# Optimization experiments

Hardware: AMD Instinct MI355X
Metric: run time of the kernel (lower is better)

The kernel has to match this reference:

```python
import jax, jax.numpy as jnp
import numpy as np

B, N, L, E, D = 16, 16384, 192, 128, 128


def setup_inputs() -> dict:
    key = jax.random.key(0)
    ks = jax.random.split(key, 16)
    s = 0.05
    return {
        "x_L_flattened": jax.random.normal(ks[0], (B, N), jnp.float32),
        "x_y_mask_flattened": jax.random.randint(ks[1], (B, N), 0, 2).astype(jnp.float32),
        "y_mask_L_flattened": jnp.zeros((B, N), jnp.float32),
        "x_y_mark": jax.random.normal(ks[2], (B, L, 1), jnp.float32),
        "variable_indices_flattened": jax.random.randint(ks[3], (B, N), 0, E),
        "time_indices_flattened": jax.random.randint(ks[4], (B, N), 0, L),
        "N_OBSERVATIONS_MAX": N,
        # learned params (stored [in, out]; torch Linear uses x @ W.T + b)
        "W_obs": jax.random.normal(ks[5], (2, D), jnp.float32) * s,
        "b_obs": jnp.zeros((D,), jnp.float32),
        "W_time": jax.random.normal(ks[6], (1, D), jnp.float32) * s,
        "b_time": jnp.zeros((D,), jnp.float32),
        "var_hyperedge_w": jax.random.normal(ks[7], (E, D), jnp.float32),
        "W_q": jax.random.normal(ks[8], (D, D), jnp.float32) * s,
        "b_q": jnp.zeros((D,), jnp.float32),
        "W_k": jax.random.normal(ks[9], (D, D), jnp.float32) * s,
        "b_k": jnp.zeros((D,), jnp.float32),
        "W_v": jax.random.normal(ks[10], (D, D), jnp.float32) * s,
        "b_v": jnp.zeros((D,), jnp.float32),
        "threshold": jnp.float32(0.5),
        "merge_coef": jnp.float32(0.5),
    }


def reference(x_L_flattened, x_y_mask_flattened, y_mask_L_flattened, x_y_mark,
              variable_indices_flattened, time_indices_flattened, N_OBSERVATIONS_MAX,
              W_obs, b_obs, W_time, b_time, var_hyperedge_w,
              W_q, b_q, W_k, b_k, W_v, b_v, threshold, merge_coef):
    mask = x_y_mask_flattened  # [B, N]
    # node features: value + (1 - mask + y_mask) channel -> [B, N, 2]
    feats = jnp.stack([x_L_flattened, 1.0 - mask + y_mask_L_flattened], axis=-1)
    # temporal incidence: node n belongs to time-edge l iff time_idx[n] == l; [B, L, N]
    ti = (time_indices_flattened[:, None, :] == jnp.arange(L)[None, :, None]).astype(jnp.float32)
    ti = ti * mask[:, None, :]
    # variable incidence: node n belongs to var-edge e iff var_idx[n] == e; [B, E, N]
    vi = (jnp.arange(E)[None, :, None] == variable_indices_flattened[:, None, :]).astype(jnp.float32)
    vi = vi * mask[:, None, :]
    # encoders
    obs = jax.nn.relu(feats @ W_obs + b_obs) * mask[..., None]          # [B, N, D]
    temp_he = jnp.sin(x_y_mark @ W_time + b_time)                        # [B, L, D]
    var_he = jax.nn.relu(jnp.broadcast_to(var_hyperedge_w, (B, E, D)))   # [B, E, D]
    # IrregularityAwareAttention over variable hyperedges with incidence as aux
    q = var_he @ W_q + b_q
    k = var_he @ W_k + b_k
    v = var_he @ W_v + b_v
    att = jnp.einsum('bed,bfd->bef', q, k) / (D ** 0.5)                  # [B, E, E]
    att_aux = jnp.einsum('ben,bfn->bef', vi, vi) / (N_OBSERVATIONS_MAX ** 0.5)
    merge = (att > threshold) & (att_aux != 0)
    att = jnp.where(merge, (1.0 - merge_coef) * att + merge_coef * att_aux, att)
    attn = jax.nn.softmax(att, axis=-1)
    out = jnp.einsum('bef,bfd->bed', attn, v)                            # [B, E, D]
    return (obs, temp_he, out, ti, vi)
```

## Files before the change

### kernel.cpp

```cpp
#include <hip/hip_runtime.h>

#define Bb 16
#define Nn 16384
#define Ll 192
#define Ee 128
#define Dd 128


#define QKV_NB   128
#define TEMP_NB  512
#define FILL_NB  2048
#define OBS_NB   2048
#define TEMP_B0  (QKV_NB)
#define FILL_B0  (TEMP_B0 + TEMP_NB)
#define OBS_B0   (FILL_B0 + FILL_NB)
#define GRID1    (OBS_B0 + OBS_NB)

#define FILL_LANES (FILL_NB * 256)
#define OBS_LANES  (OBS_NB * 256)
#define TEMP_LANES (TEMP_NB * 256)

using f4 = __attribute__((ext_vector_type(4))) float;

__global__ __launch_bounds__(256) void k_main(
    const float* __restrict__ var_w,
    const float* __restrict__ Wq, const float* __restrict__ bq,
    const float* __restrict__ Wk, const float* __restrict__ bk,
    const float* __restrict__ Wv, const float* __restrict__ bv,
    const float* __restrict__ x, const float* __restrict__ mask,
    const float* __restrict__ ymask,
    const float* __restrict__ W_obs, const float* __restrict__ b_obs,
    const float* __restrict__ mark, const float* __restrict__ Wt,
    const float* __restrict__ bt,
    float* __restrict__ zfill,
    float* __restrict__ q, float* __restrict__ kT, float* __restrict__ v,
    float* __restrict__ obs, float* __restrict__ temp)
{
    __shared__ float sh[Dd];
    const int tid = threadIdx.x;
    const unsigned bx = blockIdx.x;

    if (bx >= OBS_B0) {
        const unsigned lane = (bx - OBS_B0) * 256 + tid;
        const int d = (lane & 31) << 2;

        const float4 w0 = *reinterpret_cast<const float4*>(W_obs + d);
        const float4 w1 = *reinterpret_cast<const float4*>(W_obs + Dd + d);
        const float4 bb = *reinterpret_cast<const float4*>(b_obs + d);

        #pragma unroll 4
        for (int i = 0; i < 16; ++i) {
            const unsigned idx = lane + (unsigned)i * OBS_LANES;
            const int row = idx >> 5;

            const float m  = mask[row];
            const float xv = x[row];
            const float f1 = 1.0f - m + ymask[row];

            f4 o;
            o.x = fmaxf(fmaf(xv, w0.x, fmaf(f1, w1.x, bb.x)), 0.0f) * m;
            o.y = fmaxf(fmaf(xv, w0.y, fmaf(f1, w1.y, bb.y)), 0.0f) * m;
            o.z = fmaxf(fmaf(xv, w0.z, fmaf(f1, w1.z, bb.z)), 0.0f) * m;
            o.w = fmaxf(fmaf(xv, w0.w, fmaf(f1, w1.w, bb.w)), 0.0f) * m;
            __builtin_nontemporal_store(
                o, reinterpret_cast<f4*>(obs + ((size_t)row << 7) + d));
        }
    } else if (bx >= FILL_B0) {
        f4* p = reinterpret_cast<f4*>(zfill);
        const size_t lane = (size_t)(bx - FILL_B0) * 256 + tid;
        const f4 z = {0.0f, 0.0f, 0.0f, 0.0f};
        #pragma unroll 8
        for (int i = 0; i < 40; ++i)
            __builtin_nontemporal_store(z, p + lane + (size_t)i * FILL_LANES);
    } else if (bx >= TEMP_B0) {
        const int lane = (bx - TEMP_B0) * 256 + tid;
        #pragma unroll
        for (int i = 0; i < 3; ++i) {
            const int idx = lane + i * TEMP_LANES;
            const int d = idx & 127;
            const int r = idx >> 7;
            __builtin_nontemporal_store(sinf(fmaf(mark[r], Wt[d], bt[d])),
                                        temp + idx);
        }
    } else {
        const int e = bx;
        if (tid < Dd) sh[tid] = fmaxf(var_w[e * Dd + tid], 0.0f);
        __syncthreads();
        if (tid < Dd) {
            float aq = bq[tid], ak = bk[tid], av = bv[tid];
            #pragma unroll 4
            for (int j = 0; j < Dd; ++j) {
                const float hj = sh[j];
                aq = fmaf(hj, Wq[j * Dd + tid], aq);
                ak = fmaf(hj, Wk[j * Dd + tid], ak);
                av = fmaf(hj, Wv[j * Dd + tid], av);
            }
            q[e * Dd + tid]  = aq;
            kT[tid * Dd + e] = ak;
            v[e * Dd + tid]  = av;
        }
    }
}

__global__ __launch_bounds__(256) void k_scatter(
    const int* __restrict__ tidx, const int* __restrict__ vidx,
    const float* __restrict__ mask,
    float* __restrict__ ti, float* __restrict__ vi,
    float* __restrict__ cnt_part)
{
    __shared__ float sh[Ee];
    const int tid = threadIdx.x;
    const int g  = blockIdx.x * 256 + tid;
    const int b  = g >> 12;
    const int n4 = (g & 4095) << 2;

    const int4   t4 = *reinterpret_cast<const int4*>(tidx + b * Nn + n4);
    const int4   v4 = *reinterpret_cast<const int4*>(vidx + b * Nn + n4);
    const float4 m4 = *reinterpret_cast<const float4*>(mask + b * Nn + n4);

    if (tid < Ee) sh[tid] = 0.0f;
    __syncthreads();

    float* tib = ti + (((size_t)b * Ll) << 14);
    float* vib = vi + (((size_t)b * Ee) << 14);

    if (m4.x != 0.0f) {
        atomicAdd(&sh[v4.x], 1.0f);
        tib[((size_t)t4.x << 14) + n4]     = m4.x;
        vib[((size_t)v4.x << 14) + n4]     = m4.x;
    }
    if (m4.y != 0.0f) {
        atomicAdd(&sh[v4.y], 1.0f);
        tib[((size_t)t4.y << 14) + n4 + 1] = m4.y;
        vib[((size_t)v4.y << 14) + n4 + 1] = m4.y;
    }
    if (m4.z != 0.0f) {
        atomicAdd(&sh[v4.z], 1.0f);
        tib[((size_t)t4.z << 14) + n4 + 2] = m4.z;
        vib[((size_t)v4.z << 14) + n4 + 2] = m4.z;
    }
    if (m4.w != 0.0f) {
        atomicAdd(&sh[v4.w], 1.0f);
        tib[((size_t)t4.w << 14) + n4 + 3] = m4.w;
        vib[((size_t)v4.w << 14) + n4 + 3] = m4.w;
    }

    __syncthreads();
    if (tid < Ee) cnt_part[blockIdx.x * Ee + tid] = sh[tid];
}

__global__ __launch_bounds__(128) void k_soft(
    const float* __restrict__ q, const float* __restrict__ kT,
    const float* __restrict__ v, const float* __restrict__ cnt_part,
    const float* __restrict__ thr_p, const float* __restrict__ mc_p,
    const int* __restrict__ nobs_p, float* __restrict__ outp)
{
    __shared__ float qr[Dd];
    __shared__ float attn[Ee];
    __shared__ float red[5];
    const int b = blockIdx.x >> 7;
    const int e = blockIdx.x & 127;
    const int f = threadIdx.x;

    qr[f] = q[e * Dd + f];

    float cp = (f < 16) ? cnt_part[(b * 16 + f) * Ee + e] : 0.0f;
    #pragma unroll
    for (int off = 8; off > 0; off >>= 1) cp += __shfl_xor(cp, off);
    if (f == 0) red[4] = cp;
    __syncthreads();

    float acc0 = 0.0f;
    #pragma unroll 4
    for (int d = 0; d < Dd; ++d) acc0 = fmaf(qr[d], kT[d * Dd + f], acc0);
    float a = acc0 * 0.08838834764831845f;

    if (f == e) {
        const float c = red[4];
        const float thr = *thr_p;
        if (c != 0.0f && a > thr) {
            const float mc  = *mc_p;
            const float aux = c / sqrtf((float)(*nobs_p));
            a = (1.0f - mc) * a + mc * aux;
        }
    }

    float mx = a;
    #pragma unroll
    for (int off = 32; off > 0; off >>= 1) mx = fmaxf(mx, __shfl_xor(mx, off));
    if ((f & 63) == 0) red[f >> 6] = mx;
    __syncthreads();
    mx = fmaxf(red[0], red[1]);

    const float ex = expf(a - mx);
    float s = ex;
    #pragma unroll
    for (int off = 32; off > 0; off >>= 1) s += __shfl_xor(s, off);
    if ((f & 63) == 0) red[2 + (f >> 6)] = s;
    __syncthreads();
    s = red[2] + red[3];

    attn[f] = ex / s;
    __syncthreads();

    const int d = f;
    float acc = 0.0f;
    #pragma unroll 4
    for (int j = 0; j < Ee; ++j) acc = fmaf(attn[j], v[j * Dd + d], acc);
    outp[((size_t)(b * Ee + e) << 7) + d] = acc;
}

extern "C" void kernel_launch(void* const* d_in, const int* in_sizes, int n_in,
                              void* d_out, int out_size, void* d_ws, size_t ws_size,
                              hipStream_t stream) {
    (void)in_sizes; (void)n_in; (void)out_size; (void)ws_size;

    const float* x      = (const float*)d_in[0];
    const float* mask   = (const float*)d_in[1];
    const float* ymask  = (const float*)d_in[2];
    const float* mark   = (const float*)d_in[3];
    const int*   vidx   = (const int*)d_in[4];
    const int*   tidx   = (const int*)d_in[5];
    const int*   nobs   = (const int*)d_in[6];
    const float* W_obs  = (const float*)d_in[7];
    const float* b_obs  = (const float*)d_in[8];
    const float* W_time = (const float*)d_in[9];
    const float* b_time = (const float*)d_in[10];
    const float* var_w  = (const float*)d_in[11];
    const float* W_q    = (const float*)d_in[12];
    const float* b_q    = (const float*)d_in[13];
    const float* W_k    = (const float*)d_in[14];
    const float* b_k    = (const float*)d_in[15];
    const float* W_v    = (const float*)d_in[16];
    const float* b_v    = (const float*)d_in[17];
    const float* thr    = (const float*)d_in[18];
    const float* mc     = (const float*)d_in[19];

    float* out_base = (float*)d_out;
    float* obs  = out_base;
    float* temp = out_base + 33554432;
    float* attO = out_base + 33947648;
    float* ti   = out_base + 34209792;
    float* vi   = out_base + 84541440;

    float* ws       = (float*)d_ws;
    float* cnt_part = ws;
    float* q        = ws + 32768;
    float* kT       = ws + 49152;
    float* v        = ws + 65536;

    k_main<<<GRID1, 256, 0, stream>>>(var_w,
                                      W_q, b_q, W_k, b_k, W_v, b_v,
                                      x, mask, ymask, W_obs, b_obs,
                                      mark, W_time, b_time,
                                      ti ,
                                      q, kT, v, obs, temp);
    k_scatter<<<256, 256, 0, stream>>>(tidx, vidx, mask, ti, vi, cnt_part);
    k_soft<<<Bb * Ee, Dd, 0, stream>>>(q, kT, v, cnt_part, thr, mc, nobs, attO);
}
```

Before: 579.7 us.

## Replace zero-fill plus scatter with per-plane dense incidence writes fused into main kernel

```diff
diff --git a/kernel.cpp b/kernel.cpp
--- a/kernel.cpp
+++ b/kernel.cpp
@@ -7,40 +7,73 @@
 #define Dd 128
 
 
+#define PLN_NB   5120
+#define OBS_NB   2048
+#define TEMP_NB  512
 #define QKV_NB   128
-#define TEMP_NB  512
-#define FILL_NB  2048
-#define OBS_NB   2048
-#define TEMP_B0  (QKV_NB)
-#define FILL_B0  (TEMP_B0 + TEMP_NB)
-#define OBS_B0   (FILL_B0 + FILL_NB)
-#define GRID1    (OBS_B0 + OBS_NB)
-
-#define FILL_LANES (FILL_NB * 256)
+#define OBS_B0   (PLN_NB)
+#define TEMP_B0  (OBS_B0 + OBS_NB)
+#define QKV_B0   (TEMP_B0 + TEMP_NB)
+#define GRID1    (QKV_B0 + QKV_NB)
+
 #define OBS_LANES  (OBS_NB * 256)
 #define TEMP_LANES (TEMP_NB * 256)
 
-using f4 = __attribute__((ext_vector_type(4))) float;
-
 __global__ __launch_bounds__(256) void k_main(
-    const float* __restrict__ var_w,
+    const int* __restrict__ tidx, const int* __restrict__ vidx,
+    const float* __restrict__ mask, const float* __restrict__ var_w,
     const float* __restrict__ Wq, const float* __restrict__ bq,
     const float* __restrict__ Wk, const float* __restrict__ bk,
     const float* __restrict__ Wv, const float* __restrict__ bv,
-    const float* __restrict__ x, const float* __restrict__ mask,
-    const float* __restrict__ ymask,
+    const float* __restrict__ x, const float* __restrict__ ymask,
     const float* __restrict__ W_obs, const float* __restrict__ b_obs,
     const float* __restrict__ mark, const float* __restrict__ Wt,
     const float* __restrict__ bt,
-    float* __restrict__ zfill,
+    float* __restrict__ ti, float* __restrict__ vi,
+    float* __restrict__ cnt,
     float* __restrict__ q, float* __restrict__ kT, float* __restrict__ v,
     float* __restrict__ obs, float* __restrict__ temp)
 {
     __shared__ float sh[Dd];
+    __shared__ float rr[4];
     const int tid = threadIdx.x;
     const unsigned bx = blockIdx.x;
 
-    if (bx >= OBS_B0) {
+    if (bx < PLN_NB) {
+        const int b     = bx / 320;
+        const int pl    = bx - b * 320;
+        const bool isti = (pl < Ll);
+        const int plane = isti ? pl : pl - Ll;
+
+        const int*   ib = (isti ? tidx : vidx) + b * Nn;
+        const float* mb = mask + b * Nn;
+        float* op = isti ? (ti + (((size_t)(b * Ll + plane)) << 14))
+                         : (vi + (((size_t)(b * Ee + plane)) << 14));
+
+        float c = 0.0f;
+        #pragma unroll 4
+        for (int i = 0; i < 16; ++i) {
+            const int n4 = ((i << 8) + tid) << 2;
+            const int4   t4 = *reinterpret_cast<const int4*>(ib + n4);
+            const float4 m4 = *reinterpret_cast<const float4*>(mb + n4);
+            float4 o;
+            o.x = (t4.x == plane) ? m4.x : 0.0f;
+            o.y = (t4.y == plane) ? m4.y : 0.0f;
+            o.z = (t4.z == plane) ? m4.z : 0.0f;
+            o.w = (t4.w == plane) ? m4.w : 0.0f;
+            *reinterpret_cast<float4*>(op + n4) = o;
+            c += (o.x + o.y) + (o.z + o.w);
+        }
+
+        if (!isti) {
+            #pragma unroll
+            for (int off = 32; off > 0; off >>= 1) c += __shfl_xor(c, off);
+            if ((tid & 63) == 0) rr[tid >> 6] = c;
+            __syncthreads();
+            if (tid == 0)
+                cnt[b * Ee + plane] = (rr[0] + rr[1]) + (rr[2] + rr[3]);
+        }
+    } else if (bx < TEMP_B0) {
         const unsigned lane = (bx - OBS_B0) * 256 + tid;
         const int d = (lane & 31) << 2;
 
@@ -57,33 +90,24 @@
             const float xv = x[row];
             const float f1 = 1.0f - m + ymask[row];
 
-            f4 o;
+            float4 o;
             o.x = fmaxf(fmaf(xv, w0.x, fmaf(f1, w1.x, bb.x)), 0.0f) * m;
             o.y = fmaxf(fmaf(xv, w0.y, fmaf(f1, w1.y, bb.y)), 0.0f) * m;
             o.z = fmaxf(fmaf(xv, w0.z, fmaf(f1, w1.z, bb.z)), 0.0f) * m;
             o.w = fmaxf(fmaf(xv, w0.w, fmaf(f1, w1.w, bb.w)), 0.0f) * m;
-            __builtin_nontemporal_store(
-                o, reinterpret_cast<f4*>(obs + ((size_t)row << 7) + d));
-        }
-    } else if (bx >= FILL_B0) {
-        f4* p = reinterpret_cast<f4*>(zfill);
-        const size_t lane = (size_t)(bx - FILL_B0) * 256 + tid;
-        const f4 z = {0.0f, 0.0f, 0.0f, 0.0f};
-        #pragma unroll 8
-        for (int i = 0; i < 40; ++i)
-            __builtin_nontemporal_store(z, p + lane + (size_t)i * FILL_LANES);
-    } else if (bx >= TEMP_B0) {
+            *reinterpret_cast<float4*>(obs + ((size_t)row << 7) + d) = o;
+        }
+    } else if (bx < QKV_B0) {
         const int lane = (bx - TEMP_B0) * 256 + tid;
         #pragma unroll
         for (int i = 0; i < 3; ++i) {
             const int idx = lane + i * TEMP_LANES;
             const int d = idx & 127;
             const int r = idx >> 7;
-            __builtin_nontemporal_store(sinf(fmaf(mark[r], Wt[d], bt[d])),
-                                        temp + idx);
+            temp[idx] = sinf(fmaf(mark[r], Wt[d], bt[d]));
         }
     } else {
-        const int e = bx;
+        const int e = bx - QKV_B0;
         if (tid < Dd) sh[tid] = fmaxf(var_w[e * Dd + tid], 0.0f);
         __syncthreads();
         if (tid < Dd) {
@@ -102,72 +126,20 @@
     }
 }
 
-__global__ __launch_bounds__(256) void k_scatter(
-    const int* __restrict__ tidx, const int* __restrict__ vidx,
-    const float* __restrict__ mask,
-    float* __restrict__ ti, float* __restrict__ vi,
-    float* __restrict__ cnt_part)
-{
-    __shared__ float sh[Ee];
-    const int tid = threadIdx.x;
-    const int g  = blockIdx.x * 256 + tid;
-    const int b  = g >> 12;
-    const int n4 = (g & 4095) << 2;
-
-    const int4   t4 = *reinterpret_cast<const int4*>(tidx + b * Nn + n4);
-    const int4   v4 = *reinterpret_cast<const int4*>(vidx + b * Nn + n4);
-    const float4 m4 = *reinterpret_cast<const float4*>(mask + b * Nn + n4);
-
-    if (tid < Ee) sh[tid] = 0.0f;
-    __syncthreads();
-
-    float* tib = ti + (((size_t)b * Ll) << 14);
-    float* vib = vi + (((size_t)b * Ee) << 14);
-
-    if (m4.x != 0.0f) {
-        atomicAdd(&sh[v4.x], 1.0f);
-        tib[((size_t)t4.x << 14) + n4]     = m4.x;
-        vib[((size_t)v4.x << 14) + n4]     = m4.x;
-    }
-    if (m4.y != 0.0f) {
-        atomicAdd(&sh[v4.y], 1.0f);
-        tib[((size_t)t4.y << 14) + n4 + 1] = m4.y;
-        vib[((size_t)v4.y << 14) + n4 + 1] = m4.y;
-    }
-    if (m4.z != 0.0f) {
-        atomicAdd(&sh[v4.z], 1.0f);
-        tib[((size_t)t4.z << 14) + n4 + 2] = m4.z;
-        vib[((size_t)v4.z << 14) + n4 + 2] = m4.z;
-    }
-    if (m4.w != 0.0f) {
-        atomicAdd(&sh[v4.w], 1.0f);
-        tib[((size_t)t4.w << 14) + n4 + 3] = m4.w;
-        vib[((size_t)v4.w << 14) + n4 + 3] = m4.w;
-    }
-
-    __syncthreads();
-    if (tid < Ee) cnt_part[blockIdx.x * Ee + tid] = sh[tid];
-}
-
 __global__ __launch_bounds__(128) void k_soft(
     const float* __restrict__ q, const float* __restrict__ kT,
-    const float* __restrict__ v, const float* __restrict__ cnt_part,
+    const float* __restrict__ v, const float* __restrict__ cnt,
     const float* __restrict__ thr_p, const float* __restrict__ mc_p,
     const int* __restrict__ nobs_p, float* __restrict__ outp)
 {
     __shared__ float qr[Dd];
     __shared__ float attn[Ee];
-    __shared__ float red[5];
+    __shared__ float red[4];
     const int b = blockIdx.x >> 7;
     const int e = blockIdx.x & 127;
     const int f = threadIdx.x;
 
     qr[f] = q[e * Dd + f];
-
-    float cp = (f < 16) ? cnt_part[(b * 16 + f) * Ee + e] : 0.0f;
-    #pragma unroll
-    for (int off = 8; off > 0; off >>= 1) cp += __shfl_xor(cp, off);
-    if (f == 0) red[4] = cp;
     __syncthreads();
 
     float acc0 = 0.0f;
@@ -176,7 +148,7 @@
     float a = acc0 * 0.08838834764831845f;
 
     if (f == e) {
-        const float c = red[4];
+        const float c = cnt[b * Ee + e];
         const float thr = *thr_p;
         if (c != 0.0f && a > thr) {
             const float mc  = *mc_p;
@@ -243,18 +215,16 @@
     float* ti   = out_base + 34209792;
     float* vi   = out_base + 84541440;
 
-    float* ws       = (float*)d_ws;
-    float* cnt_part = ws;
-    float* q        = ws + 32768;
-    float* kT       = ws + 49152;
-    float* v        = ws + 65536;
-
-    k_main<<<GRID1, 256, 0, stream>>>(var_w,
+    float* ws  = (float*)d_ws;
+    float* cnt = ws;
+    float* q   = ws + 2048;
+    float* kT  = ws + 2048 + 16384;
+    float* v   = ws + 2048 + 32768;
+
+    k_main<<<GRID1, 256, 0, stream>>>(tidx, vidx, mask, var_w,
                                       W_q, b_q, W_k, b_k, W_v, b_v,
-                                      x, mask, ymask, W_obs, b_obs,
+                                      x, ymask, W_obs, b_obs,
                                       mark, W_time, b_time,
-                                      ti ,
-                                      q, kT, v, obs, temp);
-    k_scatter<<<256, 256, 0, stream>>>(tidx, vidx, mask, ti, vi, cnt_part);
-    k_soft<<<Bb * Ee, Dd, 0, stream>>>(q, kT, v, cnt_part, thr, mc, nobs, attO);
+                                      ti, vi, cnt, q, kT, v, obs, temp);
+    k_soft<<<Bb * Ee, Dd, 0, stream>>>(q, kT, v, cnt, thr, mc, nobs, attO);
 }
```

Measured after the change: 567.1 us. -2.2%, faster.
